# Performance work log

Measured on AMD Instinct MI355X. Metric: run time of the kernel, lower is better.

## Reference

```python
import jax, jax.numpy as jnp
import numpy as np

VOCAB, EMB, H, OUT = 32000, 512, 1024, 32000
SEQ, B = 512, 64

def setup_inputs() -> dict:
    key = jax.random.key(0)
    ks = jax.random.split(key, 16)
    sc = lambda *s: 1.0 / np.sqrt(s[-1])
    return {
        "x": jax.random.randint(ks[0], (B,), 0, VOCAB),
        "encoder_states": jax.random.normal(ks[1], (SEQ, B, 2 * H), jnp.float32),
        "hidden": jax.random.normal(ks[2], (1, B, H), jnp.float32),
        "cell": jax.random.normal(ks[3], (1, B, H), jnp.float32),
        "emb_table": jax.random.normal(ks[4], (VOCAB, EMB), jnp.float32),
        "energy_W": jax.random.normal(ks[5], (1, 3 * H), jnp.float32) * sc(1, 3 * H),
        "energy_b": jnp.zeros((1,), jnp.float32),
        "W_ih": jax.random.normal(ks[6], (4 * H, 2 * H + EMB), jnp.float32) * sc(1, H),
        "W_hh": jax.random.normal(ks[7], (4 * H, H), jnp.float32) * sc(1, H),
        "b_ih": jnp.zeros((4 * H,), jnp.float32),
        "b_hh": jnp.zeros((4 * H,), jnp.float32),
        "fc_W": jax.random.normal(ks[8], (OUT, H), jnp.float32) * sc(1, H),
        "fc_b": jnp.zeros((OUT,), jnp.float32),
    }

def reference(x, encoder_states, hidden, cell, emb_table, energy_W, energy_b,
              W_ih, W_hh, b_ih, b_hh, fc_W, fc_b):
    S = encoder_states.shape[0]
    emb = emb_table[x]                                     # [B, E] (dropout is identity at p=0)
    h_rep = jnp.broadcast_to(hidden, (S,) + hidden.shape[1:])   # [S, B, H]
    cat = jnp.concatenate([h_rep, encoder_states], axis=2)      # [S, B, 3H]
    energy = jax.nn.relu(jnp.einsum('sbk,ok->sbo', cat, energy_W) + energy_b)  # [S, B, 1]
    attn = jax.nn.softmax(energy[..., 0], axis=0)                # softmax over seq dim -> [S, B]
    context = jnp.einsum('sb,sbd->bd', attn, encoder_states)     # [B, 2H]
    rnn_in = jnp.concatenate([context, emb], axis=1)             # [B, 2H+E]
    gates = rnn_in @ W_ih.T + b_ih + hidden[0] @ W_hh.T + b_hh   # [B, 4H]
    i, f, g, o = jnp.split(gates, 4, axis=1)
    i, f, o = jax.nn.sigmoid(i), jax.nn.sigmoid(f), jax.nn.sigmoid(o)
    g = jnp.tanh(g)
    c_new = f * cell[0] + i * g
    h_new = o * jnp.tanh(c_new)
    preds = h_new @ fc_W.T + fc_b                                # [B, OUT]
    return preds, h_new[None], c_new[None]
```

## Files before the change

kernel.cpp:

```cpp
#include <hip/hip_runtime.h>

#define S_LEN 512
#define BATCH 64
#define HDIM  1024
#define TWOH  2048
#define EMB   512
#define KDIM  2560
#define KTOT  3584
#define VOUT  32000

#define WS_MS    64
#define WS_CTX   2112
#define WS_GP    WS_CTX
#define WS_RNNB  (WS_CTX + 64*16*2048)
#define WS_HB16  (WS_RNNB + 114688)

typedef __attribute__((ext_vector_type(8))) short bf16x8;
typedef __attribute__((ext_vector_type(4))) float f32x4;

__device__ __forceinline__ float sigmoidf_(float x) { return 1.f/(1.f+__expf(-x)); }

__device__ __forceinline__ unsigned short f2bf(float f) {
  union { float f; unsigned u; } v; v.f = f;
  return (unsigned short)((v.u + 0x7fffu + ((v.u >> 16) & 1u)) >> 16);
}

__device__ __forceinline__ bf16x8 cvt_frag(const float4& a, const float4& b) {
  bf16x8 r;
  r[0] = (short)f2bf(a.x); r[1] = (short)f2bf(a.y);
  r[2] = (short)f2bf(a.z); r[3] = (short)f2bf(a.w);
  r[4] = (short)f2bf(b.x); r[5] = (short)f2bf(b.y);
  r[6] = (short)f2bf(b.z); r[7] = (short)f2bf(b.w);
  return r;
}

__global__ __launch_bounds__(256) void k_attn(const float* __restrict__ enc,
                                              const float* __restrict__ eW,
                                              const float* __restrict__ eb,
                                              const float* __restrict__ hidden,
                                              float* __restrict__ ws_ms,
                                              float* __restrict__ ws_ctx) {
  __shared__ float lds_ms[4][2];
  __shared__ float lds_ctx[4][2048];
  const int lane  = threadIdx.x & 63;
  const int wave  = threadIdx.x >> 6;
  const int chunk = blockIdx.x;
  const int b     = blockIdx.y;

  float hba = 0.f;
  for (int k = lane; k < HDIM; k += 64) hba += hidden[b*HDIM + k] * eW[k];
#pragma unroll
  for (int st = 32; st >= 1; st >>= 1) hba += __shfl_xor(hba, st, 64);
  const float hb = hba + eb[0];

  float4 w4[8];
#pragma unroll
  for (int k = 0; k < 8; ++k)
    w4[k] = *reinterpret_cast<const float4*>(eW + HDIM + 4*lane + 256*k);

  const int s0 = chunk*32 + wave*8;
  const float* base = enc + ((size_t)(s0*BATCH + b))*TWOH + 4*lane;

  float m = 0.f, ssum = 0.f;
  float4 ctx[8];
#pragma unroll
  for (int k = 0; k < 8; ++k) ctx[k] = make_float4(0.f, 0.f, 0.f, 0.f);

  float4 va[8], vb[8];
#pragma unroll
  for (int k = 0; k < 8; ++k) va[k] = *reinterpret_cast<const float4*>(base + 256*k);

#define ATTN_STEP(VCUR, VNXT, I)                                              \
  {                                                                           \
    if ((I) < 7) {                                                            \
      const float* pn = base + (size_t)((I)+1)*BATCH*TWOH;                    \
      _Pragma("unroll")                                                       \
      for (int k = 0; k < 8; ++k)                                             \
        VNXT[k] = *reinterpret_cast<const float4*>(pn + 256*k);               \
    }                                                                         \
    float a = 0.f;                                                            \
    _Pragma("unroll")                                                         \
    for (int k = 0; k < 8; ++k)                                               \
      a += VCUR[k].x*w4[k].x + VCUR[k].y*w4[k].y +                            \
           VCUR[k].z*w4[k].z + VCUR[k].w*w4[k].w;                             \
    _Pragma("unroll")                                                         \
    for (int st = 1; st < 64; st <<= 1) a += __shfl_xor(a, st, 64);           \
    const float e = fmaxf(a + hb, 0.f);                                       \
    if (e > m) {                                                              \
      const float sc = __expf(m - e);                                         \
      ssum = ssum*sc + 1.f;                                                   \
      _Pragma("unroll")                                                       \
      for (int k = 0; k < 8; ++k) {                                           \
        ctx[k].x = fmaf(ctx[k].x, sc, VCUR[k].x);                             \
        ctx[k].y = fmaf(ctx[k].y, sc, VCUR[k].y);                             \
        ctx[k].z = fmaf(ctx[k].z, sc, VCUR[k].z);                             \
        ctx[k].w = fmaf(ctx[k].w, sc, VCUR[k].w);                             \
      }                                                                       \
      m = e;                                                                  \
    } else {                                                                  \
      const float pw = __expf(e - m);                                         \
      ssum += pw;                                                             \
      _Pragma("unroll")                                                       \
      for (int k = 0; k < 8; ++k) {                                           \
        ctx[k].x = fmaf(pw, VCUR[k].x, ctx[k].x);                             \
        ctx[k].y = fmaf(pw, VCUR[k].y, ctx[k].y);                             \
        ctx[k].z = fmaf(pw, VCUR[k].z, ctx[k].z);                             \
        ctx[k].w = fmaf(pw, VCUR[k].w, ctx[k].w);                             \
      }                                                                       \
    }                                                                         \
  }

  ATTN_STEP(va, vb, 0)
  ATTN_STEP(vb, va, 1)
  ATTN_STEP(va, vb, 2)
  ATTN_STEP(vb, va, 3)
  ATTN_STEP(va, vb, 4)
  ATTN_STEP(vb, va, 5)
  ATTN_STEP(va, vb, 6)
  ATTN_STEP(vb, va, 7)
#undef ATTN_STEP

  if (lane == 0) { lds_ms[wave][0] = m; lds_ms[wave][1] = ssum; }
  __syncthreads();
  const float M = fmaxf(fmaxf(lds_ms[0][0], lds_ms[1][0]),
                        fmaxf(lds_ms[2][0], lds_ms[3][0]));
  const float wsc = __expf(m - M);
  float ssum_c = 0.f;
#pragma unroll
  for (int w = 0; w < 4; ++w) ssum_c += __expf(lds_ms[w][0] - M) * lds_ms[w][1];
#pragma unroll
  for (int k = 0; k < 8; ++k) {
    float4 c = ctx[k];
    c.x *= wsc; c.y *= wsc; c.z *= wsc; c.w *= wsc;
    *reinterpret_cast<float4*>(&lds_ctx[wave][4*lane + 256*k]) = c;
  }
  __syncthreads();
  float* outp = ws_ctx + ((size_t)b*16 + chunk)*TWOH;
  for (int d = threadIdx.x; d < TWOH; d += 256)
    outp[d] = lds_ctx[0][d] + lds_ctx[1][d] + lds_ctx[2][d] + lds_ctx[3][d];
  if (threadIdx.x == 0) {
    ws_ms[((size_t)b*16 + chunk)*2]     = M;
    ws_ms[((size_t)b*16 + chunk)*2 + 1] = ssum_c;
  }
}

__global__ __launch_bounds__(256) void k_combine(const float* __restrict__ ws_ms,
                                                 const float* __restrict__ ws_ctx,
                                                 const float* __restrict__ hidden,
                                                 const float* __restrict__ emb_table,
                                                 const int* __restrict__ x,
                                                 unsigned short* __restrict__ rnnB) {
  const int b = blockIdx.y;
  const int k = blockIdx.x*256 + threadIdx.x;
  unsigned short* rb = rnnB + (size_t)b*KTOT;

  if (k < TWOH) {
    float mc[16], sc[16];
#pragma unroll
    for (int c = 0; c < 16; ++c) {
      mc[c] = ws_ms[(b*16 + c)*2];
      sc[c] = ws_ms[(b*16 + c)*2 + 1];
    }
    float M = mc[0];
#pragma unroll
    for (int c = 1; c < 16; ++c) M = fmaxf(M, mc[c]);
    float wc[16], Ssum = 0.f;
#pragma unroll
    for (int c = 0; c < 16; ++c) { wc[c] = __expf(mc[c] - M); Ssum += wc[c]*sc[c]; }
    const float inv = 1.f / Ssum;
    float a = 0.f;
#pragma unroll
    for (int c = 0; c < 16; ++c) a += wc[c] * ws_ctx[((size_t)b*16 + c)*TWOH + k];
    rb[k] = f2bf(a * inv);
  } else if (k < KDIM) {
    const int xb = x[b];
    rb[k] = f2bf(emb_table[(size_t)xb*EMB + (k - TWOH)]);
  } else {
    rb[k] = f2bf(hidden[b*HDIM + (k - KDIM)]);
  }
}

__global__ __launch_bounds__(256) void k_gates(const unsigned short* __restrict__ rnnB,
                                               const float* __restrict__ W_ih,
                                               const float* __restrict__ W_hh,
                                               float* __restrict__ ws_gp) {
  const int lane = threadIdx.x & 63;
  const int wave = threadIdx.x >> 6;
  const int part = blockIdx.x & 7;
  const int rg   = blockIdx.x >> 3;
  const int row0 = rg*64 + wave*16;
  const int mlo  = lane & 15;
  const int kg   = lane >> 4;
  const int j    = row0 + mlo;
  const unsigned short* rp0 = rnnB + (size_t)mlo*KTOT;

  f32x4 acc0 = {0.f,0.f,0.f,0.f}, acc1 = acc0, acc2 = acc0, acc3 = acc0;

  float4  Aa[4], Ab[4];
  bf16x8  Ba[8], Bb[8];

#define G_LOAD(AW, BB, S)                                                     \
  {                                                                           \
    const int kb0 = part*448 + (S)*64;                                        \
    const int kb1 = kb0 + 32;                                                 \
    const float* ws0 = (kb0 < KDIM) ? (W_ih + (size_t)j*KDIM + kb0 + kg*8)    \
                                    : (W_hh + (size_t)j*HDIM + (kb0-KDIM) + kg*8); \
    const float* ws1 = (kb1 < KDIM) ? (W_ih + (size_t)j*KDIM + kb1 + kg*8)    \
                                    : (W_hh + (size_t)j*HDIM + (kb1-KDIM) + kg*8); \
    AW[0] = *reinterpret_cast<const float4*>(ws0);                            \
    AW[1] = *reinterpret_cast<const float4*>(ws0 + 4);                        \
    AW[2] = *reinterpret_cast<const float4*>(ws1);                            \
    AW[3] = *reinterpret_cast<const float4*>(ws1 + 4);                        \
    const size_t ko0 = (size_t)kb0 + kg*8;                                    \
    const size_t ko1 = (size_t)kb1 + kg*8;                                    \
    BB[0] = *reinterpret_cast<const bf16x8*>(rp0 + ko0);                      \
    BB[1] = *reinterpret_cast<const bf16x8*>(rp0 + 16*KTOT + ko0);            \
    BB[2] = *reinterpret_cast<const bf16x8*>(rp0 + 32*KTOT + ko0);            \
    BB[3] = *reinterpret_cast<const bf16x8*>(rp0 + 48*KTOT + ko0);            \
    BB[4] = *reinterpret_cast<const bf16x8*>(rp0 + ko1);                      \
    BB[5] = *reinterpret_cast<const bf16x8*>(rp0 + 16*KTOT + ko1);            \
    BB[6] = *reinterpret_cast<const bf16x8*>(rp0 + 32*KTOT + ko1);            \
    BB[7] = *reinterpret_cast<const bf16x8*>(rp0 + 48*KTOT + ko1);            \
  }

#define G_COMP(AW, BB)                                                        \
  {                                                                           \
    const bf16x8 af0 = cvt_frag(AW[0], AW[1]);                                \
    const bf16x8 af1 = cvt_frag(AW[2], AW[3]);                                \
    acc0 = __builtin_amdgcn_mfma_f32_16x16x32_bf16(af0, BB[0], acc0, 0, 0, 0);\
    acc1 = __builtin_amdgcn_mfma_f32_16x16x32_bf16(af0, BB[1], acc1, 0, 0, 0);\
    acc2 = __builtin_amdgcn_mfma_f32_16x16x32_bf16(af0, BB[2], acc2, 0, 0, 0);\
    acc3 = __builtin_amdgcn_mfma_f32_16x16x32_bf16(af0, BB[3], acc3, 0, 0, 0);\
    acc0 = __builtin_amdgcn_mfma_f32_16x16x32_bf16(af1, BB[4], acc0, 0, 0, 0);\
    acc1 = __builtin_amdgcn_mfma_f32_16x16x32_bf16(af1, BB[5], acc1, 0, 0, 0);\
    acc2 = __builtin_amdgcn_mfma_f32_16x16x32_bf16(af1, BB[6], acc2, 0, 0, 0);\
    acc3 = __builtin_amdgcn_mfma_f32_16x16x32_bf16(af1, BB[7], acc3, 0, 0, 0);\
  }

  G_LOAD(Aa, Ba, 0)
  G_LOAD(Ab, Bb, 1) G_COMP(Aa, Ba)
  G_LOAD(Aa, Ba, 2) G_COMP(Ab, Bb)
  G_LOAD(Ab, Bb, 3) G_COMP(Aa, Ba)
  G_LOAD(Aa, Ba, 4) G_COMP(Ab, Bb)
  G_LOAD(Ab, Bb, 5) G_COMP(Aa, Ba)
  G_LOAD(Aa, Ba, 6) G_COMP(Ab, Bb)
  G_COMP(Aa, Ba)
#undef G_LOAD
#undef G_COMP

  const int mbase = row0 + kg*4;
#define G_ST(ACC, N)                                                          \
  {                                                                           \
    _Pragma("unroll")                                                         \
    for (int jj = 0; jj < 4; ++jj)                                            \
      ws_gp[((size_t)part*4096 + mbase + jj)*64 + ((N)*16 + mlo)] = ACC[jj];  \
  }
  G_ST(acc0, 0) G_ST(acc1, 1) G_ST(acc2, 2) G_ST(acc3, 3)
#undef G_ST
}

__global__ __launch_bounds__(256) void k_lstm(const float* __restrict__ ws_gp,
                                              const float* __restrict__ b_ih,
                                              const float* __restrict__ b_hh,
                                              const float* __restrict__ cell,
                                              float* __restrict__ out_h,
                                              float* __restrict__ out_c,
                                              unsigned short* __restrict__ hB) {
  const int id = blockIdx.x*256 + threadIdx.x;
  const int h = id >> 6, b = id & 63;
  float g[4];
#pragma unroll
  for (int gg = 0; gg < 4; ++gg) {
    const int j = gg*1024 + h;
    float v = b_ih[j] + b_hh[j];
#pragma unroll
    for (int p = 0; p < 8; ++p) v += ws_gp[((size_t)p*4096 + j)*64 + b];
    g[gg] = v;
  }
  const float iv = sigmoidf_(g[0]);
  const float fv = sigmoidf_(g[1]);
  const float gv = tanhf(g[2]);
  const float ov = sigmoidf_(g[3]);
  const float cold = cell[b*HDIM + h];
  const float cn = fmaf(fv, cold, iv*gv);
  const float hn = ov * tanhf(cn);
  out_h[b*HDIM + h] = hn;
  out_c[b*HDIM + h] = cn;
  hB[(size_t)b*HDIM + h] = f2bf(hn);
}

__global__ __launch_bounds__(256) void k_fc(const unsigned short* __restrict__ hB,
                                            const float* __restrict__ fc_W,
                                            const float* __restrict__ fc_b,
                                            float* __restrict__ preds) {
  __shared__ unsigned short lds_a[2][64*64];
  const int tid  = threadIdx.x;
  const int lane = tid & 63;
  const int wave = tid >> 6;
  const int row0b = blockIdx.x * 64;
  const int mlo  = lane & 15;
  const int kg   = lane >> 4;
  const int srow = tid >> 4;
  const int scol = (tid & 15) * 4;

  const unsigned short* hp = hB + (size_t)mlo*HDIM + kg*8;

  f32x4 acc0 = {0.f,0.f,0.f,0.f}, acc1 = acc0, acc2 = acc0, acc3 = acc0;
  float4 st[4];

#define FC_GLOAD(C)                                                           \
  _Pragma("unroll")                                                           \
  for (int jj = 0; jj < 4; ++jj)                                              \
    st[jj] = *reinterpret_cast<const float4*>(                                \
        fc_W + (size_t)(row0b + srow + jj*16)*HDIM + (C)*64 + scol);

#define FC_SWRITE(BUF)                                                        \
  _Pragma("unroll")                                                           \
  for (int jj = 0; jj < 4; ++jj) {                                            \
    const int r = srow + jj*16;                                               \
    unsigned short tmp[4];                                                    \
    tmp[0] = f2bf(st[jj].x); tmp[1] = f2bf(st[jj].y);                         \
    tmp[2] = f2bf(st[jj].z); tmp[3] = f2bf(st[jj].w);                         \
    const int boff = r*128 + ((scol*2) ^ ((r & 7) << 4));                     \
    *reinterpret_cast<uint2*>(reinterpret_cast<char*>(lds_a[BUF]) + boff) =   \
        *reinterpret_cast<const uint2*>(tmp);                                 \
  }

  FC_GLOAD(0)
  FC_SWRITE(0)
  __syncthreads();

  int cur = 0;
  const int arow = wave*16 + mlo;
  const int abase = arow*128;
  const int asw  = (arow & 7) << 4;

  for (int c = 0; c < 16; ++c) {
    if (c < 15) FC_GLOAD(c+1)

    const bf16x8 af0 = *reinterpret_cast<const bf16x8*>(
        reinterpret_cast<const char*>(lds_a[cur]) + abase + ((kg*16) ^ asw));
    const bf16x8 af1 = *reinterpret_cast<const bf16x8*>(
        reinterpret_cast<const char*>(lds_a[cur]) + abase + ((64 + kg*16) ^ asw));

    const int K0 = c*64;
    const bf16x8 b00 = *reinterpret_cast<const bf16x8*>(hp + K0);
    const bf16x8 b10 = *reinterpret_cast<const bf16x8*>(hp + 16*HDIM + K0);
    const bf16x8 b20 = *reinterpret_cast<const bf16x8*>(hp + 32*HDIM + K0);
    const bf16x8 b30 = *reinterpret_cast<const bf16x8*>(hp + 48*HDIM + K0);
    const bf16x8 b01 = *reinterpret_cast<const bf16x8*>(hp + K0 + 32);
    const bf16x8 b11 = *reinterpret_cast<const bf16x8*>(hp + 16*HDIM + K0 + 32);
    const bf16x8 b21 = *reinterpret_cast<const bf16x8*>(hp + 32*HDIM + K0 + 32);
    const bf16x8 b31 = *reinterpret_cast<const bf16x8*>(hp + 48*HDIM + K0 + 32);

    acc0 = __builtin_amdgcn_mfma_f32_16x16x32_bf16(af0, b00, acc0, 0, 0, 0);
    acc1 = __builtin_amdgcn_mfma_f32_16x16x32_bf16(af0, b10, acc1, 0, 0, 0);
    acc2 = __builtin_amdgcn_mfma_f32_16x16x32_bf16(af0, b20, acc2, 0, 0, 0);
    acc3 = __builtin_amdgcn_mfma_f32_16x16x32_bf16(af0, b30, acc3, 0, 0, 0);
    acc0 = __builtin_amdgcn_mfma_f32_16x16x32_bf16(af1, b01, acc0, 0, 0, 0);
    acc1 = __builtin_amdgcn_mfma_f32_16x16x32_bf16(af1, b11, acc1, 0, 0, 0);
    acc2 = __builtin_amdgcn_mfma_f32_16x16x32_bf16(af1, b21, acc2, 0, 0, 0);
    acc3 = __builtin_amdgcn_mfma_f32_16x16x32_bf16(af1, b31, acc3, 0, 0, 0);

    if (c < 15) FC_SWRITE(cur ^ 1)
    __syncthreads();
    cur ^= 1;
  }
#undef FC_GLOAD
#undef FC_SWRITE

  const int mbase = row0b + wave*16 + kg*4;
  const float4 bias = make_float4(fc_b[mbase], fc_b[mbase+1],
                                  fc_b[mbase+2], fc_b[mbase+3]);
#define FC_STORE(ACC, N)                                                      \
  {                                                                           \
    float4 stv = make_float4(ACC[0] + bias.x, ACC[1] + bias.y,                \
                             ACC[2] + bias.z, ACC[3] + bias.w);               \
    *reinterpret_cast<float4*>(preds + (size_t)((N)*16 + mlo)*VOUT + mbase) = stv; \
  }
  FC_STORE(acc0, 0) FC_STORE(acc1, 1) FC_STORE(acc2, 2) FC_STORE(acc3, 3)
#undef FC_STORE
}

extern "C" void kernel_launch(void* const* d_in, const int* in_sizes, int n_in,
                              void* d_out, int out_size, void* d_ws, size_t ws_size,
                              hipStream_t stream) {
  const int*   x      = (const int*)  d_in[0];
  const float* enc    = (const float*)d_in[1];
  const float* hidden = (const float*)d_in[2];
  const float* cell   = (const float*)d_in[3];
  const float* embt   = (const float*)d_in[4];
  const float* eW     = (const float*)d_in[5];
  const float* eb     = (const float*)d_in[6];
  const float* W_ih   = (const float*)d_in[7];
  const float* W_hh   = (const float*)d_in[8];
  const float* b_ih   = (const float*)d_in[9];
  const float* b_hh   = (const float*)d_in[10];
  const float* fc_W   = (const float*)d_in[11];
  const float* fc_b   = (const float*)d_in[12];

  float* out   = (float*)d_out;
  float* preds = out;
  float* out_h = out + (size_t)BATCH*VOUT;
  float* out_c = out_h + BATCH*HDIM;
  float* ws    = (float*)d_ws;
  unsigned short* rnnB = (unsigned short*)(ws + WS_RNNB);
  unsigned short* hB   = (unsigned short*)(ws + WS_HB16);

  k_attn<<<dim3(16, 64), 256, 0, stream>>>(enc, eW, eb, hidden, ws + WS_MS, ws + WS_CTX);
  k_combine<<<dim3(14, 64), 256, 0, stream>>>(ws + WS_MS, ws + WS_CTX, hidden, embt, x, rnnB);
  k_gates<<<512, 256, 0, stream>>>(rnnB, W_ih, W_hh, ws + WS_GP);
  k_lstm<<<256, 256, 0, stream>>>(ws + WS_GP, b_ih, b_hh, cell, out_h, out_c, hB);
  k_fc<<<500, 256, 0, stream>>>(hB, fc_W, fc_b, preds);
}
```

Baseline: 139.0 us.

## Stage gate weights through swizzled double-buffered LDS in k_gates

```diff
diff --git a/kernel.cpp b/kernel.cpp
--- a/kernel.cpp
+++ b/kernel.cpp
@@ -23,15 +23,6 @@
 __device__ __forceinline__ unsigned short f2bf(float f) {
   union { float f; unsigned u; } v; v.f = f;
   return (unsigned short)((v.u + 0x7fffu + ((v.u >> 16) & 1u)) >> 16);
-}
-
-__device__ __forceinline__ bf16x8 cvt_frag(const float4& a, const float4& b) {
-  bf16x8 r;
-  r[0] = (short)f2bf(a.x); r[1] = (short)f2bf(a.y);
-  r[2] = (short)f2bf(a.z); r[3] = (short)f2bf(a.w);
-  r[4] = (short)f2bf(b.x); r[5] = (short)f2bf(b.y);
-  r[6] = (short)f2bf(b.z); r[7] = (short)f2bf(b.w);
-  return r;
 }
 
 __global__ __launch_bounds__(256) void k_attn(const float* __restrict__ enc,
@@ -184,71 +175,92 @@
                                                const float* __restrict__ W_ih,
                                                const float* __restrict__ W_hh,
                                                float* __restrict__ ws_gp) {
-  const int lane = threadIdx.x & 63;
-  const int wave = threadIdx.x >> 6;
+  __shared__ unsigned short lds_a[2][64*64];
+  const int tid  = threadIdx.x;
+  const int lane = tid & 63;
+  const int wave = tid >> 6;
   const int part = blockIdx.x & 7;
   const int rg   = blockIdx.x >> 3;
-  const int row0 = rg*64 + wave*16;
+  const int j0   = rg*64;
   const int mlo  = lane & 15;
   const int kg   = lane >> 4;
-  const int j    = row0 + mlo;
+  const int srow = tid >> 4;
+  const int scol = (tid & 15) * 4;
+
   const unsigned short* rp0 = rnnB + (size_t)mlo*KTOT;
 
   f32x4 acc0 = {0.f,0.f,0.f,0.f}, acc1 = acc0, acc2 = acc0, acc3 = acc0;
-
-  float4  Aa[4], Ab[4];
-  bf16x8  Ba[8], Bb[8];
-
-#define G_LOAD(AW, BB, S)                                                     \
+  float4 st[4];
+
+#define G_GLOAD(C)                                                            \
   {                                                                           \
-    const int kb0 = part*448 + (S)*64;                                        \
-    const int kb1 = kb0 + 32;                                                 \
-    const float* ws0 = (kb0 < KDIM) ? (W_ih + (size_t)j*KDIM + kb0 + kg*8)    \
-                                    : (W_hh + (size_t)j*HDIM + (kb0-KDIM) + kg*8); \
-    const float* ws1 = (kb1 < KDIM) ? (W_ih + (size_t)j*KDIM + kb1 + kg*8)    \
-                                    : (W_hh + (size_t)j*HDIM + (kb1-KDIM) + kg*8); \
-    AW[0] = *reinterpret_cast<const float4*>(ws0);                            \
-    AW[1] = *reinterpret_cast<const float4*>(ws0 + 4);                        \
-    AW[2] = *reinterpret_cast<const float4*>(ws1);                            \
-    AW[3] = *reinterpret_cast<const float4*>(ws1 + 4);                        \
-    const size_t ko0 = (size_t)kb0 + kg*8;                                    \
-    const size_t ko1 = (size_t)kb1 + kg*8;                                    \
-    BB[0] = *reinterpret_cast<const bf16x8*>(rp0 + ko0);                      \
-    BB[1] = *reinterpret_cast<const bf16x8*>(rp0 + 16*KTOT + ko0);            \
-    BB[2] = *reinterpret_cast<const bf16x8*>(rp0 + 32*KTOT + ko0);            \
-    BB[3] = *reinterpret_cast<const bf16x8*>(rp0 + 48*KTOT + ko0);            \
-    BB[4] = *reinterpret_cast<const bf16x8*>(rp0 + ko1);                      \
-    BB[5] = *reinterpret_cast<const bf16x8*>(rp0 + 16*KTOT + ko1);            \
-    BB[6] = *reinterpret_cast<const bf16x8*>(rp0 + 32*KTOT + ko1);            \
-    BB[7] = *reinterpret_cast<const bf16x8*>(rp0 + 48*KTOT + ko1);            \
-  }
-
-#define G_COMP(AW, BB)                                                        \
-  {                                                                           \
-    const bf16x8 af0 = cvt_frag(AW[0], AW[1]);                                \
-    const bf16x8 af1 = cvt_frag(AW[2], AW[3]);                                \
-    acc0 = __builtin_amdgcn_mfma_f32_16x16x32_bf16(af0, BB[0], acc0, 0, 0, 0);\
-    acc1 = __builtin_amdgcn_mfma_f32_16x16x32_bf16(af0, BB[1], acc1, 0, 0, 0);\
-    acc2 = __builtin_amdgcn_mfma_f32_16x16x32_bf16(af0, BB[2], acc2, 0, 0, 0);\
-    acc3 = __builtin_amdgcn_mfma_f32_16x16x32_bf16(af0, BB[3], acc3, 0, 0, 0);\
-    acc0 = __builtin_amdgcn_mfma_f32_16x16x32_bf16(af1, BB[4], acc0, 0, 0, 0);\
-    acc1 = __builtin_amdgcn_mfma_f32_16x16x32_bf16(af1, BB[5], acc1, 0, 0, 0);\
-    acc2 = __builtin_amdgcn_mfma_f32_16x16x32_bf16(af1, BB[6], acc2, 0, 0, 0);\
-    acc3 = __builtin_amdgcn_mfma_f32_16x16x32_bf16(af1, BB[7], acc3, 0, 0, 0);\
-  }
-
-  G_LOAD(Aa, Ba, 0)
-  G_LOAD(Ab, Bb, 1) G_COMP(Aa, Ba)
-  G_LOAD(Aa, Ba, 2) G_COMP(Ab, Bb)
-  G_LOAD(Ab, Bb, 3) G_COMP(Aa, Ba)
-  G_LOAD(Aa, Ba, 4) G_COMP(Ab, Bb)
-  G_LOAD(Ab, Bb, 5) G_COMP(Aa, Ba)
-  G_LOAD(Aa, Ba, 6) G_COMP(Ab, Bb)
-  G_COMP(Aa, Ba)
-#undef G_LOAD
-#undef G_COMP
-
-  const int mbase = row0 + kg*4;
+    const int kb = part*448 + (C)*64;                                         \
+    _Pragma("unroll")                                                         \
+    for (int jj = 0; jj < 4; ++jj) {                                          \
+      const int r = j0 + srow + jj*16;                                        \
+      const float* wrow = (kb < KDIM)                                         \
+          ? (W_ih + (size_t)r*KDIM + kb + scol)                               \
+          : (W_hh + (size_t)r*HDIM + (kb - KDIM) + scol);                     \
+      st[jj] = *reinterpret_cast<const float4*>(wrow);                        \
+    }                                                                         \
+  }
+
+#define G_SWRITE(BUF)                                                         \
+  _Pragma("unroll")                                                           \
+  for (int jj = 0; jj < 4; ++jj) {                                            \
+    const int r = srow + jj*16;                                               \
+    unsigned short tmp[4];                                                    \
+    tmp[0] = f2bf(st[jj].x); tmp[1] = f2bf(st[jj].y);                         \
+    tmp[2] = f2bf(st[jj].z); tmp[3] = f2bf(st[jj].w);                         \
+    const int boff = r*128 + ((scol*2) ^ ((r & 7) << 4));                     \
+    *reinterpret_cast<uint2*>(reinterpret_cast<char*>(lds_a[BUF]) + boff) =   \
+        *reinterpret_cast<const uint2*>(tmp);                                 \
+  }
+
+  G_GLOAD(0)
+  G_SWRITE(0)
+  __syncthreads();
+
+  int cur = 0;
+  const int arow = wave*16 + mlo;
+  const int abase = arow*128;
+  const int asw  = (arow & 7) << 4;
+
+  for (int c = 0; c < 7; ++c) {
+    if (c < 6) G_GLOAD(c+1)
+
+    const bf16x8 af0 = *reinterpret_cast<const bf16x8*>(
+        reinterpret_cast<const char*>(lds_a[cur]) + abase + ((kg*16) ^ asw));
+    const bf16x8 af1 = *reinterpret_cast<const bf16x8*>(
+        reinterpret_cast<const char*>(lds_a[cur]) + abase + ((64 + kg*16) ^ asw));
+
+    const size_t K0 = (size_t)part*448 + c*64 + kg*8;
+    const bf16x8 b00 = *reinterpret_cast<const bf16x8*>(rp0 + K0);
+    const bf16x8 b10 = *reinterpret_cast<const bf16x8*>(rp0 + 16*KTOT + K0);
+    const bf16x8 b20 = *reinterpret_cast<const bf16x8*>(rp0 + 32*KTOT + K0);
+    const bf16x8 b30 = *reinterpret_cast<const bf16x8*>(rp0 + 48*KTOT + K0);
+    const bf16x8 b01 = *reinterpret_cast<const bf16x8*>(rp0 + K0 + 32);
+    const bf16x8 b11 = *reinterpret_cast<const bf16x8*>(rp0 + 16*KTOT + K0 + 32);
+    const bf16x8 b21 = *reinterpret_cast<const bf16x8*>(rp0 + 32*KTOT + K0 + 32);
+    const bf16x8 b31 = *reinterpret_cast<const bf16x8*>(rp0 + 48*KTOT + K0 + 32);
+
+    acc0 = __builtin_amdgcn_mfma_f32_16x16x32_bf16(af0, b00, acc0, 0, 0, 0);
+    acc1 = __builtin_amdgcn_mfma_f32_16x16x32_bf16(af0, b10, acc1, 0, 0, 0);
+    acc2 = __builtin_amdgcn_mfma_f32_16x16x32_bf16(af0, b20, acc2, 0, 0, 0);
+    acc3 = __builtin_amdgcn_mfma_f32_16x16x32_bf16(af0, b30, acc3, 0, 0, 0);
+    acc0 = __builtin_amdgcn_mfma_f32_16x16x32_bf16(af1, b01, acc0, 0, 0, 0);
+    acc1 = __builtin_amdgcn_mfma_f32_16x16x32_bf16(af1, b11, acc1, 0, 0, 0);
+    acc2 = __builtin_amdgcn_mfma_f32_16x16x32_bf16(af1, b21, acc2, 0, 0, 0);
+    acc3 = __builtin_amdgcn_mfma_f32_16x16x32_bf16(af1, b31, acc3, 0, 0, 0);
+
+    if (c < 6) G_SWRITE(cur ^ 1)
+    __syncthreads();
+    cur ^= 1;
+  }
+#undef G_GLOAD
+#undef G_SWRITE
+
+  const int mbase = j0 + wave*16 + kg*4;
 #define G_ST(ACC, N)                                                          \
   {                                                                           \
     _Pragma("unroll")                                                         \
```

Result: no change. 137.4 us (median of 2 runs) (-1.1%).
